# Kernel tuning notes

Measured on AMD Instinct MI355X. Metric: run time of the kernel, lower is better.

The kernel has to match this reference:

```python
import jax, jax.numpy as jnp
import numpy as np

B, S, H, I, E, K = 1, 2048, 1024, 512, 16, 4


def setup_inputs() -> dict:
    key = jax.random.key(0)
    k0, k1, k2, k3, k4, k5 = jax.random.split(key, 6)
    hidden_states = jax.random.normal(k0, (B, S, H), jnp.float32)
    T = B * S
    topk_idx = jax.random.randint(k1, (T, K), 0, E, dtype=jnp.int32)
    raw = jax.random.uniform(k2, (T, K), jnp.float32)
    topk_weight = raw / jnp.sum(raw, axis=-1, keepdims=True)  # normalized top-k gate weights
    scale = 0.02
    w_gate = jax.random.normal(k3, (E, H, I), jnp.float32) * scale
    w_up = jax.random.normal(k4, (E, H, I), jnp.float32) * scale
    w_down = jax.random.normal(k5, (E, I, H), jnp.float32) * scale
    return {
        "hidden_states": hidden_states,
        "topk_idx": topk_idx,
        "topk_weight": topk_weight,
        "w_gate": w_gate,
        "w_up": w_up,
        "w_down": w_down,
    }


def reference(hidden_states, topk_idx, topk_weight, w_gate, w_up, w_down):
    # hidden_states: [B,S,H]; topk_idx/topk_weight: [T,K]; w_*: [E,H,I]/[E,I,H]
    b, s, h = hidden_states.shape
    t = b * s
    e = w_gate.shape[0]
    x = hidden_states.reshape(t, h)
    # routing_weights.scatter_(1, topk_idx, topk_weight)
    routing_weights = jnp.zeros((t, e), x.dtype).at[
        jnp.arange(t)[:, None], topk_idx
    ].set(topk_weight)
    # per-expert gated MLP over all tokens (math identical to masked dispatch:
    # tokens with routing weight 0 contribute nothing)
    g = jnp.einsum("th,ehi->eti", x, w_gate)  # [E,T,I]
    u = jnp.einsum("th,ehi->eti", x, w_up)
    d = jnp.einsum("eti,eih->eth", jax.nn.silu(g) * u, w_down)  # [E,T,H]
    out = jnp.einsum("eth,te->th", d, routing_weights)  # weighted combine
    return out.reshape(b, s, h)
```

## Files before the change

### kernel.cpp

```cpp
#include <hip/hip_runtime.h>
#include <hip/hip_bf16.h>
#include <stdint.h>

#define HH 1024
#define II 512
#define EE 16
#define TT 2048
#define KTOP 4
#define PP (TT * KTOP)
#define MAXROWS 12288

typedef unsigned short u16;
typedef unsigned int u32;
typedef __attribute__((ext_vector_type(8))) short short8;
typedef __attribute__((ext_vector_type(4))) float f32x4;
typedef __attribute__((ext_vector_type(4))) unsigned short u16x4;
typedef __attribute__((ext_vector_type(8))) unsigned short u16x8;
typedef __attribute__((ext_vector_type(4))) unsigned int u32x4;

__device__ __forceinline__ u16 f2bf(float f) {
  union { float f; unsigned u; } v; v.f = f;
  unsigned r = v.u + 0x7fffu + ((v.u >> 16) & 1u);
  return (u16)(r >> 16);
}
__device__ __forceinline__ float bf2f(u16 b) {
  union { unsigned u; float f; } v; v.u = ((unsigned)b) << 16; return v.f;
}

__device__ __forceinline__ void gld16(const u16* g, u16* l) {
  __builtin_amdgcn_global_load_lds(
      (const __attribute__((address_space(1))) unsigned int*)g,
      (__attribute__((address_space(3))) unsigned int*)l, 16, 0, 0);
}

union PLds {
  int s_e[PP];
  u32 t32[128][68];
};

__global__ __launch_bounds__(1024) void prep_fused(
    const float* __restrict__ x, const int* __restrict__ tidx,
    const float* __restrict__ tw,
    const float* __restrict__ wg, const float* __restrict__ wu,
    const float* __restrict__ wd,
    u16* __restrict__ xb, u16* __restrict__ WgT, u16* __restrict__ WuT,
    u16* __restrict__ WdT,
    int* __restrict__ perm, float* __restrict__ wt, int* __restrict__ rowof,
    int* __restrict__ tile_e, int* __restrict__ tile_r,
    int* __restrict__ ntiles) {
  __shared__ PLds L;
  __shared__ int whist[16][16];
  __shared__ int wbase[16][16];
  __shared__ int pad_lo[EE], pad_hi[EE];

  const int bid = blockIdx.x;
  const int tid = threadIdx.x;

  if (bid == 0) {
    const int lane = tid & 63;
    const int wv = tid >> 6;

#pragma unroll
    for (int i = 0; i < 2; i++) {
      const int t = tid + i * 1024;
      const int4 v = ((const int4*)tidx)[t];
      const bool v0 = (v.x != v.y) && (v.x != v.z) && (v.x != v.w);
      const bool v1 = (v.y != v.z) && (v.y != v.w);
      const bool v2 = (v.z != v.w);
      L.s_e[t * 4 + 0] = v.x | (v0 ? 16 : 0);
      L.s_e[t * 4 + 1] = v.y | (v1 ? 16 : 0);
      L.s_e[t * 4 + 2] = v.z | (v2 ? 16 : 0);
      L.s_e[t * 4 + 3] = v.w | 16;
    }
    __syncthreads();

    int h0, h1, h2, h3, h4, h5, h6, h7, h8, h9, h10, h11, h12, h13, h14, h15;
    h0=h1=h2=h3=h4=h5=h6=h7=h8=h9=h10=h11=h12=h13=h14=h15=0;
    const unsigned long long ltm = (1ull << lane) - 1ull;
    for (int c = 0; c < 8; c++) {
      const int p = (wv << 9) + (c << 6) + lane;
      const int se = L.s_e[p];
      const int e = se & 15;
      const bool valid = (se & 16) != 0;
      int rank = 0;
#define RANK_STEP(J, HJ)                                            \
      {                                                             \
        unsigned long long m = __ballot(valid && (e == J));         \
        if (valid && (e == J)) rank = HJ + __popcll(m & ltm);       \
        HJ += __popcll(m);                                          \
      }
      RANK_STEP(0, h0)  RANK_STEP(1, h1)  RANK_STEP(2, h2)  RANK_STEP(3, h3)
      RANK_STEP(4, h4)  RANK_STEP(5, h5)  RANK_STEP(6, h6)  RANK_STEP(7, h7)
      RANK_STEP(8, h8)  RANK_STEP(9, h9)  RANK_STEP(10, h10) RANK_STEP(11, h11)
      RANK_STEP(12, h12) RANK_STEP(13, h13) RANK_STEP(14, h14) RANK_STEP(15, h15)
#undef RANK_STEP
      if (valid) L.s_e[p] = se | (rank << 16);
    }
    if (lane == 0) {
      whist[wv][0] = h0;   whist[wv][1] = h1;   whist[wv][2] = h2;   whist[wv][3] = h3;
      whist[wv][4] = h4;   whist[wv][5] = h5;   whist[wv][6] = h6;   whist[wv][7] = h7;
      whist[wv][8] = h8;   whist[wv][9] = h9;   whist[wv][10] = h10; whist[wv][11] = h11;
      whist[wv][12] = h12; whist[wv][13] = h13; whist[wv][14] = h14; whist[wv][15] = h15;
    }
    __syncthreads();

    if (tid == 0) {
      int off = 0, nt = 0;
      for (int j = 0; j < EE; j++) {
        int tot = 0;
        for (int w = 0; w < 16; w++) { wbase[w][j] = off + tot; tot += whist[w][j]; }
        const int cap = (tot + 127) & ~127;
        pad_lo[j] = off + tot;
        pad_hi[j] = off + cap;
        for (int m0 = 0; m0 < cap; m0 += 128) { tile_e[nt] = j; tile_r[nt] = off + m0; nt++; }
        off += cap;
      }
      *ntiles = nt;
    }
    __syncthreads();

#pragma unroll
    for (int i = 0; i < 8; i++) {
      const int p = i * 1024 + tid;
      const int se = L.s_e[p];
      int pos = -1;
      if (se & 16) {
        const int e = se & 15;
        const int r = se >> 16;
        pos = wbase[p >> 9][e] + r;
        perm[pos] = p >> 2;
        wt[pos] = tw[p];
      }
      rowof[p] = pos;
    }
    for (int j = 0; j < EE; j++) {
      const int lo = pad_lo[j], hi = pad_hi[j];
      for (int i = lo + tid; i < hi; i += 1024) {
        perm[i] = 0;
        wt[i] = 0.f;
      }
    }
    return;
  }

  if (bid <= 128) {
    const int base = ((bid - 1) * 1024 + tid) * 16;
    f32x4 v0 = *(const f32x4*)(x + base);
    f32x4 v1 = *(const f32x4*)(x + base + 4);
    f32x4 v2 = *(const f32x4*)(x + base + 8);
    f32x4 v3 = *(const f32x4*)(x + base + 12);
    u16x8 o0 = { f2bf(v0[0]), f2bf(v0[1]), f2bf(v0[2]), f2bf(v0[3]),
                 f2bf(v1[0]), f2bf(v1[1]), f2bf(v1[2]), f2bf(v1[3]) };
    u16x8 o1 = { f2bf(v2[0]), f2bf(v2[1]), f2bf(v2[2]), f2bf(v2[3]),
                 f2bf(v3[0]), f2bf(v3[1]), f2bf(v3[2]), f2bf(v3[3]) };
    *(u16x8*)(xb + base) = o0;
    *(u16x8*)(xb + base + 8) = o1;
    return;
  }

  const int pb = bid - 129;
  const int matsel = pb >> 9;
  const int within = pb & 511;
  const int zz = within >> 5;
  const int sub = within & 31;
  const float* src; u16* dst; int R, C, xi, yi;
  if (matsel == 0)      { src = wg; dst = WgT; R = HH; C = II; xi = sub & 3; yi = sub >> 2; }
  else if (matsel == 1) { src = wu; dst = WuT; R = HH; C = II; xi = sub & 3; yi = sub >> 2; }
  else                  { src = wd; dst = WdT; R = II; C = HH; xi = sub & 7; yi = sub >> 3; }
  const size_t mat = (size_t)zz * R * C;
  const int r0 = yi * 128, c0 = xi * 128;

  const int rp = tid >> 4, cq8 = (tid & 15) * 8;
  const float* sp = src + mat + (size_t)(r0 + 2 * rp) * C + c0 + cq8;
  const f32x4 a0 = *(const f32x4*)(sp);
  const f32x4 a1 = *(const f32x4*)(sp + 4);
  const f32x4 b0 = *(const f32x4*)(sp + C);
  const f32x4 b1 = *(const f32x4*)(sp + C + 4);

  const int key = tid & 15;
  const int rpx = rp ^ ((key & 7) << 3) ^ (((key >> 2) & 1) << 2);
#pragma unroll
  for (int j = 0; j < 4; j++)
    L.t32[cq8 + j][rpx] = (u32)f2bf(a0[j]) | ((u32)f2bf(b0[j]) << 16);
#pragma unroll
  for (int j = 0; j < 4; j++)
    L.t32[cq8 + 4 + j][rpx] = (u32)f2bf(a1[j]) | ((u32)f2bf(b1[j]) << 16);
  __syncthreads();

  const int c = tid >> 3, q = tid & 7;
  const int rkey = c >> 3;
  const int qbase = (q ^ (rkey & 7)) * 8;
  const int b2 = ((rkey >> 2) & 1) * 4;
  u32x4 v0, v1;
#pragma unroll
  for (int j = 0; j < 4; j++) v0[j] = L.t32[c][qbase + b2 + j];
#pragma unroll
  for (int j = 0; j < 4; j++) v1[j] = L.t32[c][qbase + (b2 ^ 4) + j];
  u16* dp = dst + mat + (size_t)(c0 + c) * R + r0 + q * 16;
  *(u32x4*)(dp) = v0;
  *(u32x4*)(dp + 8) = v1;
}

__global__ __launch_bounds__(256) void gemm1_kernel(
    const u16* __restrict__ xb, const u16* __restrict__ WgT, const u16* __restrict__ WuT,
    const int* __restrict__ perm, const float* __restrict__ wt,
    const int* __restrict__ tile_e, const int* __restrict__ tile_r,
    const int* __restrict__ ntiles, u16* __restrict__ ACT) {
  const int tileid = blockIdx.y;
  if (tileid >= *ntiles) return;
  const int e = tile_e[tileid];
  const int row0 = tile_r[tileid];
  const int n0 = blockIdx.x * 64;

  __shared__ __align__(16) u16 As[128 * 64];
  __shared__ __align__(16) u16 Gs[64 * 64];
  __shared__ __align__(16) u16 Us[64 * 64];

  const int tid = threadIdx.x;
  const int lane = tid & 63;
  const int wid = tid >> 6;
  const int wm = wid >> 1, wn = wid & 1;
  const int fr = lane & 15, fq = lane >> 4;

  const int lrow = lane >> 3;
  const int sc8 = ((lane & 7) ^ lrow) * 8;

  const u16* gA[4]; u16* lA[4];
#pragma unroll
  for (int j = 0; j < 4; j++) {
    const int trow = j * 32 + wid * 8 + lrow;
    gA[j] = xb + (size_t)perm[row0 + trow] * HH + sc8;
    lA[j] = As + (j * 4 + wid) * 512;
  }
  const u16 *gG[2], *gU[2];
  u16 *lG[2], *lU[2];
#pragma unroll
  for (int j = 0; j < 2; j++) {
    const int nrow = j * 32 + wid * 8 + lrow;
    gG[j] = WgT + ((size_t)e * II + n0 + nrow) * HH + sc8;
    gU[j] = WuT + ((size_t)e * II + n0 + nrow) * HH + sc8;
    lG[j] = Gs + (j * 4 + wid) * 512;
    lU[j] = Us + (j * 4 + wid) * 512;
  }

  f32x4 accg[4][2], accu[4][2];
  const f32x4 vz = {0.f, 0.f, 0.f, 0.f};
#pragma unroll
  for (int m = 0; m < 4; m++)
#pragma unroll
    for (int n = 0; n < 2; n++) { accg[m][n] = vz; accu[m][n] = vz; }

  for (int k0 = 0; k0 < HH; k0 += 64) {
    __syncthreads();
#pragma unroll
    for (int j = 0; j < 4; j++) gld16(gA[j] + k0, lA[j]);
#pragma unroll
    for (int j = 0; j < 2; j++) { gld16(gG[j] + k0, lG[j]); gld16(gU[j] + k0, lU[j]); }
    __syncthreads();

#pragma unroll
    for (int ks = 0; ks < 2; ks++) {
      short8 af[4], bg[2], bu[2];
#pragma unroll
      for (int m = 0; m < 4; m++) {
        const int r = wm * 64 + m * 16 + fr;
        af[m] = *(const short8*)(&As[r * 64 + (((ks * 4 + fq) ^ (r & 7)) * 8)]);
      }
#pragma unroll
      for (int n = 0; n < 2; n++) {
        const int r = wn * 32 + n * 16 + fr;
        bg[n] = *(const short8*)(&Gs[r * 64 + (((ks * 4 + fq) ^ (r & 7)) * 8)]);
        bu[n] = *(const short8*)(&Us[r * 64 + (((ks * 4 + fq) ^ (r & 7)) * 8)]);
      }
#pragma unroll
      for (int m = 0; m < 4; m++)
#pragma unroll
        for (int n = 0; n < 2; n++) {
          accg[m][n] = __builtin_amdgcn_mfma_f32_16x16x32_bf16(af[m], bg[n], accg[m][n], 0, 0, 0);
          accu[m][n] = __builtin_amdgcn_mfma_f32_16x16x32_bf16(af[m], bu[n], accu[m][n], 0, 0, 0);
        }
    }
  }

#pragma unroll
  for (int m = 0; m < 4; m++) {
    const int rbase = wm * 64 + m * 16 + fq * 4;
#pragma unroll
    for (int j = 0; j < 4; j++) {
      const int rloc = rbase + j;
      const float w = wt[row0 + rloc];
#pragma unroll
      for (int n = 0; n < 2; n++) {
        const float g = accg[m][n][j];
        const float u = accu[m][n][j];
        const float s = g / (1.f + __expf(-g));
        ACT[(size_t)(row0 + rloc) * II + n0 + (wn * 32 + n * 16 + fr)] = f2bf(s * u * w);
      }
    }
  }
}

__global__ __launch_bounds__(256) void gemm2_kernel(
    const u16* __restrict__ ACT, const u16* __restrict__ WdT,
    const int* __restrict__ tile_e, const int* __restrict__ tile_r,
    const int* __restrict__ ntiles, u16* __restrict__ D) {
  const int tileid = blockIdx.y;
  if (tileid >= *ntiles) return;
  const int e = tile_e[tileid];
  const int row0 = tile_r[tileid];
  const int n0 = blockIdx.x * 128;

  __shared__ __align__(16) u16 As[128 * 64];
  __shared__ __align__(16) u16 Bs[128 * 64];

  const int tid = threadIdx.x;
  const int lane = tid & 63;
  const int wid = tid >> 6;
  const int wm = wid >> 1, wn = wid & 1;
  const int fr = lane & 15, fq = lane >> 4;

  const int lrow = lane >> 3;
  const int sc8 = ((lane & 7) ^ lrow) * 8;

  const u16 *gA[4], *gB[4];
  u16 *lA[4], *lB[4];
#pragma unroll
  for (int j = 0; j < 4; j++) {
    const int trow = j * 32 + wid * 8 + lrow;
    gA[j] = ACT + (size_t)(row0 + trow) * II + sc8;
    gB[j] = WdT + ((size_t)e * HH + n0 + trow) * II + sc8;
    lA[j] = As + (j * 4 + wid) * 512;
    lB[j] = Bs + (j * 4 + wid) * 512;
  }

  f32x4 acc[4][4];
  const f32x4 vz = {0.f, 0.f, 0.f, 0.f};
#pragma unroll
  for (int m = 0; m < 4; m++)
#pragma unroll
    for (int n = 0; n < 4; n++) acc[m][n] = vz;

  for (int k0 = 0; k0 < II; k0 += 64) {
    __syncthreads();
#pragma unroll
    for (int j = 0; j < 4; j++) { gld16(gA[j] + k0, lA[j]); gld16(gB[j] + k0, lB[j]); }
    __syncthreads();

#pragma unroll
    for (int ks = 0; ks < 2; ks++) {
      short8 af[4], bf[4];
#pragma unroll
      for (int m = 0; m < 4; m++) {
        const int r = wm * 64 + m * 16 + fr;
        af[m] = *(const short8*)(&As[r * 64 + (((ks * 4 + fq) ^ (r & 7)) * 8)]);
      }
#pragma unroll
      for (int n = 0; n < 4; n++) {
        const int r = wn * 64 + n * 16 + fr;
        bf[n] = *(const short8*)(&Bs[r * 64 + (((ks * 4 + fq) ^ (r & 7)) * 8)]);
      }
#pragma unroll
      for (int m = 0; m < 4; m++)
#pragma unroll
        for (int n = 0; n < 4; n++)
          acc[m][n] = __builtin_amdgcn_mfma_f32_16x16x32_bf16(af[m], bf[n], acc[m][n], 0, 0, 0);
    }
  }

#pragma unroll
  for (int m = 0; m < 4; m++) {
    const int rbase = wm * 64 + m * 16 + fq * 4;
#pragma unroll
    for (int j = 0; j < 4; j++) {
      u16* dp = D + (size_t)(row0 + rbase + j) * HH + n0 + wn * 64 + fr;
#pragma unroll
      for (int n = 0; n < 4; n++)
        dp[n * 16] = f2bf(acc[m][n][j]);
    }
  }
}

__global__ __launch_bounds__(256) void combine_kernel(
    const u16* __restrict__ D, const int* __restrict__ rowof,
    float* __restrict__ out) {
  const int t = blockIdx.x;
  const int h = threadIdx.x * 4;
  const int4 r4 = ((const int4*)rowof)[t];
  float a0 = 0.f, a1 = 0.f, a2 = 0.f, a3 = 0.f;
#define ACCUM(R)                                                     \
  if ((R) >= 0) {                                                    \
    u16x4 d = *(const u16x4*)(D + (size_t)(R) * HH + h);             \
    a0 += bf2f(d[0]); a1 += bf2f(d[1]); a2 += bf2f(d[2]); a3 += bf2f(d[3]); \
  }
  ACCUM(r4.x) ACCUM(r4.y) ACCUM(r4.z) ACCUM(r4.w)
#undef ACCUM
  float4 o = { a0, a1, a2, a3 };
  *(float4*)(out + (size_t)t * HH + h) = o;
}

extern "C" void kernel_launch(void* const* d_in, const int* in_sizes, int n_in,
                              void* d_out, int out_size, void* d_ws, size_t ws_size,
                              hipStream_t stream) {
  const float* x = (const float*)d_in[0];
  const int* tidx = (const int*)d_in[1];
  const float* tw = (const float*)d_in[2];
  const float* wg = (const float*)d_in[3];
  const float* wu = (const float*)d_in[4];
  const float* wd = (const float*)d_in[5];
  float* out = (float*)d_out;

  char* ws = (char*)d_ws;
  int* ntiles = (int*)(ws + 0);
  int* tile_e = (int*)(ws + 1024);
  int* tile_r = (int*)(ws + 2048);
  int* perm = (int*)(ws + 4096);
  float* wt = (float*)(ws + 53248);
  int* rowof = (int*)(ws + 102400);
  u16* xb = (u16*)(ws + 262144);
  u16* WgT = (u16*)(ws + 4456448);
  u16* WuT = (u16*)(ws + 21233664);
  u16* WdT = (u16*)(ws + 38010880);
  u16* ACT = (u16*)(ws + 54788096);
  u16* D = (u16*)(ws + 4456448);

  prep_fused<<<1665, 1024, 0, stream>>>(x, tidx, tw, wg, wu, wd,
                                        xb, WgT, WuT, WdT,
                                        perm, wt, rowof, tile_e, tile_r, ntiles);
  gemm1_kernel<<<dim3(II / 64, 80), 256, 0, stream>>>(xb, WgT, WuT, perm, wt,
                                                      tile_e, tile_r, ntiles, ACT);
  gemm2_kernel<<<dim3(HH / 128, 80), 256, 0, stream>>>(ACT, WdT,
                                                       tile_e, tile_r, ntiles, D);
  combine_kernel<<<TT, 256, 0, stream>>>(D, rowof, out);
}
```

Before: 79.37 us.

## Move down-proj weight transpose into gemm1 launch and merge gate/up transpose blocks

The bf16 transpose of w_down moves out of the prep kernel and into extra blocks of the gemm1 launch (blockIdx.y >= 80), so it can overlap with the first expert GEMM. Its tiles are 128x64, and each block handles two row halves. The prep kernel's gate and up transposes now share one block per tile, using a double LDS buffer so the loads of both matrices are issued together. This removes a third of the prep blocks and aims to hide the w_down conversion behind gemm1 compute. In exchange, gemm1 uses a shared LDS union and carries extra branching, and gemm2 still depends on WdT being complete, which the kernel ordering guarantees.

```diff
diff --git a/kernel.cpp b/kernel.cpp
--- a/kernel.cpp
+++ b/kernel.cpp
@@ -26,6 +26,9 @@
 __device__ __forceinline__ float bf2f(u16 b) {
   union { unsigned u; float f; } v; v.u = ((unsigned)b) << 16; return v.f;
 }
+__device__ __forceinline__ u32 packbf(float lo, float hi) {
+  return (u32)f2bf(lo) | ((u32)f2bf(hi) << 16);
+}
 
 __device__ __forceinline__ void gld16(const u16* g, u16* l) {
   __builtin_amdgcn_global_load_lds(
@@ -35,16 +38,14 @@
 
 union PLds {
   int s_e[PP];
-  u32 t32[128][68];
+  u32 t32[2][128][68];
 };
 
 __global__ __launch_bounds__(1024) void prep_fused(
     const float* __restrict__ x, const int* __restrict__ tidx,
     const float* __restrict__ tw,
     const float* __restrict__ wg, const float* __restrict__ wu,
-    const float* __restrict__ wd,
     u16* __restrict__ xb, u16* __restrict__ WgT, u16* __restrict__ WuT,
-    u16* __restrict__ WdT,
     int* __restrict__ perm, float* __restrict__ wt, int* __restrict__ rowof,
     int* __restrict__ tile_e, int* __restrict__ tile_r,
     int* __restrict__ ntiles) {
@@ -159,64 +160,142 @@
   }
 
   const int pb = bid - 129;
-  const int matsel = pb >> 9;
-  const int within = pb & 511;
-  const int zz = within >> 5;
-  const int sub = within & 31;
-  const float* src; u16* dst; int R, C, xi, yi;
-  if (matsel == 0)      { src = wg; dst = WgT; R = HH; C = II; xi = sub & 3; yi = sub >> 2; }
-  else if (matsel == 1) { src = wu; dst = WuT; R = HH; C = II; xi = sub & 3; yi = sub >> 2; }
-  else                  { src = wd; dst = WdT; R = II; C = HH; xi = sub & 7; yi = sub >> 3; }
-  const size_t mat = (size_t)zz * R * C;
+  const int zz = pb >> 5;
+  const int sub = pb & 31;
+  const int xi = sub & 3, yi = sub >> 2;
+  const size_t mat = (size_t)zz * HH * II;
   const int r0 = yi * 128, c0 = xi * 128;
 
   const int rp = tid >> 4, cq8 = (tid & 15) * 8;
-  const float* sp = src + mat + (size_t)(r0 + 2 * rp) * C + c0 + cq8;
-  const f32x4 a0 = *(const f32x4*)(sp);
-  const f32x4 a1 = *(const f32x4*)(sp + 4);
-  const f32x4 b0 = *(const f32x4*)(sp + C);
-  const f32x4 b1 = *(const f32x4*)(sp + C + 4);
+  const size_t soff = mat + (size_t)(r0 + 2 * rp) * II + c0 + cq8;
+  const float* sp0 = wg + soff;
+  const float* sp1 = wu + soff;
+  const f32x4 a0 = *(const f32x4*)(sp0);
+  const f32x4 a1 = *(const f32x4*)(sp0 + 4);
+  const f32x4 b0 = *(const f32x4*)(sp0 + II);
+  const f32x4 b1 = *(const f32x4*)(sp0 + II + 4);
+  const f32x4 e0 = *(const f32x4*)(sp1);
+  const f32x4 e1 = *(const f32x4*)(sp1 + 4);
+  const f32x4 g0 = *(const f32x4*)(sp1 + II);
+  const f32x4 g1 = *(const f32x4*)(sp1 + II + 4);
+  __builtin_amdgcn_sched_barrier(0);
 
   const int key = tid & 15;
   const int rpx = rp ^ ((key & 7) << 3) ^ (((key >> 2) & 1) << 2);
-#pragma unroll
-  for (int j = 0; j < 4; j++)
-    L.t32[cq8 + j][rpx] = (u32)f2bf(a0[j]) | ((u32)f2bf(b0[j]) << 16);
-#pragma unroll
-  for (int j = 0; j < 4; j++)
-    L.t32[cq8 + 4 + j][rpx] = (u32)f2bf(a1[j]) | ((u32)f2bf(b1[j]) << 16);
-  __syncthreads();
-
   const int c = tid >> 3, q = tid & 7;
   const int rkey = c >> 3;
-  const int qbase = (q ^ (rkey & 7)) * 8;
+  const int qb = (q ^ (rkey & 7)) * 8;
   const int b2 = ((rkey >> 2) & 1) * 4;
-  u32x4 v0, v1;
-#pragma unroll
-  for (int j = 0; j < 4; j++) v0[j] = L.t32[c][qbase + b2 + j];
-#pragma unroll
-  for (int j = 0; j < 4; j++) v1[j] = L.t32[c][qbase + (b2 ^ 4) + j];
-  u16* dp = dst + mat + (size_t)(c0 + c) * R + r0 + q * 16;
-  *(u32x4*)(dp) = v0;
-  *(u32x4*)(dp + 8) = v1;
+  const size_t doff = mat + (size_t)(c0 + c) * HH + r0 + q * 16;
+
+#pragma unroll
+  for (int j = 0; j < 4; j++) L.t32[0][cq8 + j][rpx] = packbf(a0[j], b0[j]);
+#pragma unroll
+  for (int j = 0; j < 4; j++) L.t32[0][cq8 + 4 + j][rpx] = packbf(a1[j], b1[j]);
+  __syncthreads();
+#pragma unroll
+  for (int j = 0; j < 4; j++) L.t32[1][cq8 + j][rpx] = packbf(e0[j], g0[j]);
+#pragma unroll
+  for (int j = 0; j < 4; j++) L.t32[1][cq8 + 4 + j][rpx] = packbf(e1[j], g1[j]);
+  {
+    u32x4 v0, v1;
+#pragma unroll
+    for (int j = 0; j < 4; j++) v0[j] = L.t32[0][c][qb + b2 + j];
+#pragma unroll
+    for (int j = 0; j < 4; j++) v1[j] = L.t32[0][c][qb + (b2 ^ 4) + j];
+    u16* dp = WgT + doff;
+    *(u32x4*)(dp) = v0;
+    *(u32x4*)(dp + 8) = v1;
+  }
+  __syncthreads();
+  {
+    u32x4 v0, v1;
+#pragma unroll
+    for (int j = 0; j < 4; j++) v0[j] = L.t32[1][c][qb + b2 + j];
+#pragma unroll
+    for (int j = 0; j < 4; j++) v1[j] = L.t32[1][c][qb + (b2 ^ 4) + j];
+    u16* dp = WuT + doff;
+    *(u32x4*)(dp) = v0;
+    *(u32x4*)(dp + 8) = v1;
+  }
 }
 
 __global__ __launch_bounds__(256) void gemm1_kernel(
     const u16* __restrict__ xb, const u16* __restrict__ WgT, const u16* __restrict__ WuT,
+    const float* __restrict__ wd, u16* __restrict__ WdT,
     const int* __restrict__ perm, const float* __restrict__ wt,
     const int* __restrict__ tile_e, const int* __restrict__ tile_r,
     const int* __restrict__ ntiles, u16* __restrict__ ACT) {
+  __shared__ __align__(16) u16 SMEM[16384];
+  const int tid = threadIdx.x;
+
+  if (blockIdx.y >= 80) {
+    const int pb = (blockIdx.y - 80) * 8 + blockIdx.x;
+    const int zz = pb >> 6;
+    const int sub = pb & 63;
+    const int r0 = (sub >> 4) * 128;
+    const int c0 = (sub & 15) * 64;
+    const size_t mat = (size_t)zz * II * HH;
+    u32 (*T32)[68] = (u32(*)[68])SMEM;
+
+    const int rpA = tid >> 3;
+    const int cq8 = (tid & 7) * 8;
+    const float* spA = wd + mat + (size_t)(r0 + 2 * rpA) * HH + c0 + cq8;
+    const float* spB = spA + (size_t)64 * HH;
+    const f32x4 a0 = *(const f32x4*)(spA);
+    const f32x4 a1 = *(const f32x4*)(spA + 4);
+    const f32x4 b0 = *(const f32x4*)(spA + HH);
+    const f32x4 b1 = *(const f32x4*)(spA + HH + 4);
+    const f32x4 e0 = *(const f32x4*)(spB);
+    const f32x4 e1 = *(const f32x4*)(spB + 4);
+    const f32x4 g0 = *(const f32x4*)(spB + HH);
+    const f32x4 g1 = *(const f32x4*)(spB + HH + 4);
+    __builtin_amdgcn_sched_barrier(0);
+
+    const int key = tid & 7;
+    const int sw = ((key & 7) << 3) ^ (((key >> 2) & 1) << 2);
+    const int rpxA = rpA ^ sw;
+    const int rpxB = (rpA + 32) ^ sw;
+#pragma unroll
+    for (int j = 0; j < 4; j++) T32[cq8 + j][rpxA] = packbf(a0[j], b0[j]);
+#pragma unroll
+    for (int j = 0; j < 4; j++) T32[cq8 + 4 + j][rpxA] = packbf(a1[j], b1[j]);
+#pragma unroll
+    for (int j = 0; j < 4; j++) T32[cq8 + j][rpxB] = packbf(e0[j], g0[j]);
+#pragma unroll
+    for (int j = 0; j < 4; j++) T32[cq8 + 4 + j][rpxB] = packbf(e1[j], g1[j]);
+    __syncthreads();
+
+    const int c = tid >> 2;
+    const int q2 = tid & 3;
+    const int rkey = c >> 3;
+    const int b2 = ((rkey >> 2) & 1) * 4;
+#pragma unroll
+    for (int pass = 0; pass < 2; pass++) {
+      const int o = q2 + pass * 4;
+      const int qb = (o ^ (rkey & 7)) * 8;
+      u32x4 v0, v1;
+#pragma unroll
+      for (int j = 0; j < 4; j++) v0[j] = T32[c][qb + b2 + j];
+#pragma unroll
+      for (int j = 0; j < 4; j++) v1[j] = T32[c][qb + (b2 ^ 4) + j];
+      u16* dp = WdT + mat + (size_t)(c0 + c) * II + r0 + o * 16;
+      *(u32x4*)(dp) = v0;
+      *(u32x4*)(dp + 8) = v1;
+    }
+    return;
+  }
+
   const int tileid = blockIdx.y;
   if (tileid >= *ntiles) return;
   const int e = tile_e[tileid];
   const int row0 = tile_r[tileid];
   const int n0 = blockIdx.x * 64;
 
-  __shared__ __align__(16) u16 As[128 * 64];
-  __shared__ __align__(16) u16 Gs[64 * 64];
-  __shared__ __align__(16) u16 Us[64 * 64];
-
-  const int tid = threadIdx.x;
+  u16* const As = SMEM;
+  u16* const Gs = SMEM + 8192;
+  u16* const Us = SMEM + 12288;
+
   const int lane = tid & 63;
   const int wid = tid >> 6;
   const int wm = wid >> 1, wn = wid & 1;
@@ -423,11 +502,11 @@
   u16* ACT = (u16*)(ws + 54788096);
   u16* D = (u16*)(ws + 4456448);
 
-  prep_fused<<<1665, 1024, 0, stream>>>(x, tidx, tw, wg, wu, wd,
-                                        xb, WgT, WuT, WdT,
-                                        perm, wt, rowof, tile_e, tile_r, ntiles);
-  gemm1_kernel<<<dim3(II / 64, 80), 256, 0, stream>>>(xb, WgT, WuT, perm, wt,
-                                                      tile_e, tile_r, ntiles, ACT);
+  prep_fused<<<641, 1024, 0, stream>>>(x, tidx, tw, wg, wu,
+                                       xb, WgT, WuT,
+                                       perm, wt, rowof, tile_e, tile_r, ntiles);
+  gemm1_kernel<<<dim3(8, 208), 256, 0, stream>>>(xb, WgT, WuT, wd, WdT, perm, wt,
+                                                 tile_e, tile_r, ntiles, ACT);
   gemm2_kernel<<<dim3(HH / 128, 80), 256, 0, stream>>>(ACT, WdT,
                                                        tile_e, tile_r, ntiles, D);
   combine_kernel<<<TT, 256, 0, stream>>>(D, rowof, out);
```

After: 84.18 us. +6.1%, slower.
